# Kernel optimization log

Measured on AMD Instinct MI355X. Metric: run time of the kernel, lower is better.

Reference implementation:

```python
import jax, jax.numpy as jnp
import numpy as np

H = 1024      # hidden_size
V = 50257     # output_size (vocab)
L = 100       # max_length


def setup_inputs() -> dict:
    key = jax.random.key(0)
    ks = jax.random.split(key, 14)
    s = 0.02
    return {
        "token": jax.random.randint(ks[0], (1,), 0, V),
        "hidden": jax.random.normal(ks[1], (1, 1, H), jnp.float32),
        "encoder_outputs": jax.random.normal(ks[2], (L, H), jnp.float32),
        "embedding": jax.random.normal(ks[3], (V, H), jnp.float32) * s,
        "attn_w": jax.random.normal(ks[4], (L, 2 * H), jnp.float32) * s,
        "attn_b": jnp.zeros((L,), jnp.float32),
        "comb_w": jax.random.normal(ks[5], (H, 2 * H), jnp.float32) * s,
        "comb_b": jnp.zeros((H,), jnp.float32),
        "w_ih": jax.random.normal(ks[6], (3 * H, H), jnp.float32) * s,
        "w_hh": jax.random.normal(ks[7], (3 * H, H), jnp.float32) * s,
        "b_ih": jnp.zeros((3 * H,), jnp.float32),
        "b_hh": jnp.zeros((3 * H,), jnp.float32),
        "out_w": jax.random.normal(ks[8], (V, H), jnp.float32) * s,
        "out_b": jnp.zeros((V,), jnp.float32),
    }


def reference(token, hidden, encoder_outputs, embedding, attn_w, attn_b,
              comb_w, comb_b, w_ih, w_hh, b_ih, b_hh, out_w, out_b):
    # embedding lookup; dropout is identity in eval mode
    emb = embedding[token]                                   # [1, H]
    h0 = hidden[0]                                           # [1, H]
    # attention over encoder positions
    attn_in = jnp.concatenate([emb, h0], axis=1)             # [1, 2H]
    attn_weights = jax.nn.softmax(attn_in @ attn_w.T + attn_b, axis=1)  # [1, L]
    attn_applied = attn_weights @ encoder_outputs            # [1, H]
    # combine + relu
    x = jnp.concatenate([emb, attn_applied], axis=1) @ comb_w.T + comb_b  # [1, H]
    x = jax.nn.relu(x)
    # single GRU cell step (PyTorch gate order: r, z, n)
    gi = x @ w_ih.T + b_ih                                   # [1, 3H]
    gh = h0 @ w_hh.T + b_hh                                  # [1, 3H]
    ir, iz, in_ = jnp.split(gi, 3, axis=1)
    hr, hz, hn = jnp.split(gh, 3, axis=1)
    r = jax.nn.sigmoid(ir + hr)
    z = jax.nn.sigmoid(iz + hz)
    n = jnp.tanh(in_ + r * hn)
    h_new = (1.0 - z) * n + z * h0                           # [1, H]
    # output projection + log_softmax
    output = jax.nn.log_softmax(h_new @ out_w.T + out_b, axis=1)  # [1, V]
    return output, h_new[None], attn_weights
```

## Files before the change

### kernel.cpp

```cpp
#include <hip/hip_runtime.h>
#include <hip/hip_bf16.h>

#define H 1024
#define V 50257
#define L 100
#define NPART 1024


__device__ __forceinline__ float block_reduce_sum_256(float v, float* sbuf4) {
    #pragma unroll
    for (int off = 32; off > 0; off >>= 1)
        v += __shfl_down(v, off, 64);
    int lane = threadIdx.x & 63;
    int wid  = threadIdx.x >> 6;
    __syncthreads();
    if (lane == 0) sbuf4[wid] = v;
    __syncthreads();
    return sbuf4[0] + sbuf4[1] + sbuf4[2] + sbuf4[3];
}


__global__ void k1_logits_gh(const int* token, const float* hidden, const float* embedding,
                             const float* attn_w, const float* attn_b,
                             const float* w_hh, const float* b_hh,
                             float* ws_log, float* ws_gh) {
    __shared__ float sbuf[4];
    int b = blockIdx.x;
    if (b < L) {
        int tok = token[0];
        const float* emb = embedding + (size_t)tok * H;
        const float* wrow = attn_w + (size_t)b * (2 * H);
        float acc = 0.f;
        for (int k = threadIdx.x; k < 2 * H; k += 256) {
            float inv = (k < H) ? emb[k] : hidden[k - H];
            acc += inv * wrow[k];
        }
        float s = block_reduce_sum_256(acc, sbuf);
        if (threadIdx.x == 0) ws_log[b] = s + attn_b[b];
    } else {
        int rb = b - L;
        float4 hv = ((const float4*)hidden)[threadIdx.x];
        #pragma unroll
        for (int i = 0; i < 4; i++) {
            int r = rb * 4 + i;
            const float4* wr = (const float4*)(w_hh + (size_t)r * H);
            float4 w = wr[threadIdx.x];
            float acc = w.x * hv.x + w.y * hv.y + w.z * hv.z + w.w * hv.w;
            float s = block_reduce_sum_256(acc, sbuf);
            if (threadIdx.x == 0) ws_gh[r] = s + b_hh[r];
        }
    }
}


__global__ void k2_softmax_apply(const float* ws_log, const float* enc,
                                 float* ws_app, float* out_attnw) {
    __shared__ float wsm[L];
    if (threadIdx.x < L) wsm[threadIdx.x] = ws_log[threadIdx.x];
    __syncthreads();
    float m = -1e30f;
    for (int l = 0; l < L; l++) m = fmaxf(m, wsm[l]);
    float s = 0.f;
    for (int l = 0; l < L; l++) s += expf(wsm[l] - m);
    __syncthreads();
    if (threadIdx.x < L) wsm[threadIdx.x] = expf(wsm[threadIdx.x] - m) / s;
    __syncthreads();
    int h = blockIdx.x * 256 + threadIdx.x;
    float acc = 0.f;
    for (int l = 0; l < L; l++) acc += wsm[l] * enc[l * H + h];
    ws_app[h] = acc;
    if (blockIdx.x == 0 && threadIdx.x < L) out_attnw[threadIdx.x] = wsm[threadIdx.x];
}


__global__ void k3_combine(const int* token, const float* embedding, const float* ws_app,
                           const float* comb_w, const float* comb_b, float* ws_x) {
    __shared__ float sbuf[4];
    int tok = token[0];
    const float* emb = embedding + (size_t)tok * H;
    float4 e = ((const float4*)emb)[threadIdx.x];
    float4 a = ((const float4*)ws_app)[threadIdx.x];
    for (int r = blockIdx.x; r < H; r += gridDim.x) {
        const float4* wr = (const float4*)(comb_w + (size_t)r * (2 * H));
        float4 w0 = wr[threadIdx.x];
        float4 w1 = wr[256 + threadIdx.x];
        float acc = w0.x * e.x + w0.y * e.y + w0.z * e.z + w0.w * e.w
                  + w1.x * a.x + w1.y * a.y + w1.z * a.z + w1.w * a.w;
        float s = block_reduce_sum_256(acc, sbuf);
        if (threadIdx.x == 0) ws_x[r] = fmaxf(s + comb_b[r], 0.0f);
    }
}


__global__ void k4_gi(const float* ws_x, const float* w_ih, const float* b_ih, float* ws_gi) {
    __shared__ float sbuf[4];
    float4 xv = ((const float4*)ws_x)[threadIdx.x];
    for (int r = blockIdx.x; r < 3 * H; r += gridDim.x) {
        const float4* wr = (const float4*)(w_ih + (size_t)r * H);
        float4 w = wr[threadIdx.x];
        float acc = w.x * xv.x + w.y * xv.y + w.z * xv.z + w.w * xv.w;
        float s = block_reduce_sum_256(acc, sbuf);
        if (threadIdx.x == 0) ws_gi[r] = s + b_ih[r];
    }
}


__global__ void k5_gates(const float* ws_gi, const float* ws_gh, const float* hidden,
                         float* out_h, float* ws_hn) {
    int h = blockIdx.x * 256 + threadIdx.x;
    float ir = ws_gi[h], iz = ws_gi[H + h], in_ = ws_gi[2 * H + h];
    float hr = ws_gh[h], hz = ws_gh[H + h], hn = ws_gh[2 * H + h];
    float r = 1.f / (1.f + expf(-(ir + hr)));
    float z = 1.f / (1.f + expf(-(iz + hz)));
    float n = tanhf(in_ + r * hn);
    float h0 = hidden[h];
    float v = (1.f - z) * n + z * h0;
    out_h[h] = v;
    ws_hn[h] = v;
}


__global__ void k6_outproj(const float* hn, const float* out_w, const float* out_b,
                           float* out_logits, float* ws_pm, float* ws_ps) {
    __shared__ float sm[4], ss[4];
    int lane = threadIdx.x & 63;
    int wv   = threadIdx.x >> 6;
    const float4* h4 = (const float4*)hn;
    float4 h0 = h4[lane], h1 = h4[lane + 64], h2 = h4[lane + 128], h3 = h4[lane + 192];
    float m = -1e30f, s = 0.f;
    int wid = blockIdx.x * 4 + wv;
    for (int r = wid; r < V; r += NPART * 4) {
        const float4* wr = (const float4*)(out_w + (size_t)r * H);
        float4 a = wr[lane], b = wr[lane + 64], c = wr[lane + 128], d = wr[lane + 192];
        float acc = a.x * h0.x + a.y * h0.y + a.z * h0.z + a.w * h0.w
                  + b.x * h1.x + b.y * h1.y + b.z * h1.z + b.w * h1.w
                  + c.x * h2.x + c.y * h2.y + c.z * h2.z + c.w * h2.w
                  + d.x * h3.x + d.y * h3.y + d.z * h3.z + d.w * h3.w;
        #pragma unroll
        for (int off = 32; off > 0; off >>= 1) acc += __shfl_down(acc, off, 64);
        if (lane == 0) {
            float lg = acc + out_b[r];
            out_logits[r] = lg;
            float nm = fmaxf(m, lg);
            s = s * expf(m - nm) + expf(lg - nm);
            m = nm;
        }
    }
    if (lane == 0) { sm[wv] = m; ss[wv] = s; }
    __syncthreads();
    if (threadIdx.x == 0) {
        m = sm[0]; s = ss[0];
        for (int i = 1; i < 4; i++) {
            float nm = fmaxf(m, sm[i]);
            s = s * expf(m - nm) + ss[i] * expf(sm[i] - nm);
            m = nm;
        }
        ws_pm[blockIdx.x] = m;
        ws_ps[blockIdx.x] = s;
    }
}


__global__ void k7_finalize(const float* ws_pm, const float* ws_ps, float* out) {
    __shared__ float sm[4], ss[4], fm, fs;
    int t = threadIdx.x;
    float m = -1e30f, s = 0.f;
    for (int i = t; i < NPART; i += 256) {
        float pm = ws_pm[i], ps = ws_ps[i];
        float nm = fmaxf(m, pm);
        s = s * expf(m - nm) + ps * expf(pm - nm);
        m = nm;
    }
    #pragma unroll
    for (int off = 32; off > 0; off >>= 1) {
        float om = __shfl_down(m, off, 64);
        float os = __shfl_down(s, off, 64);
        float nm = fmaxf(m, om);
        s = s * expf(m - nm) + os * expf(om - nm);
        m = nm;
    }
    int lane = t & 63, wv = t >> 6;
    if (lane == 0) { sm[wv] = m; ss[wv] = s; }
    __syncthreads();
    if (t == 0) {
        m = sm[0]; s = ss[0];
        for (int i = 1; i < 4; i++) {
            float nm = fmaxf(m, sm[i]);
            s = s * expf(m - nm) + ss[i] * expf(sm[i] - nm);
            m = nm;
        }
        fm = m; fs = logf(s);
    }
    __syncthreads();
    float M = fm, LS = fs;
    for (int v = blockIdx.x * 256 + t; v < V; v += gridDim.x * 256)
        out[v] = out[v] - M - LS;
}


extern "C" void kernel_launch(void* const* d_in, const int* in_sizes, int n_in,
                              void* d_out, int out_size, void* d_ws, size_t ws_size,
                              hipStream_t stream) {
    const int*   token     = (const int*)d_in[0];
    const float* hidden    = (const float*)d_in[1];
    const float* enc       = (const float*)d_in[2];
    const float* embedding = (const float*)d_in[3];
    const float* attn_w    = (const float*)d_in[4];
    const float* attn_b    = (const float*)d_in[5];
    const float* comb_w    = (const float*)d_in[6];
    const float* comb_b    = (const float*)d_in[7];
    const float* w_ih      = (const float*)d_in[8];
    const float* w_hh      = (const float*)d_in[9];
    const float* b_ih      = (const float*)d_in[10];
    const float* b_hh      = (const float*)d_in[11];
    const float* out_w     = (const float*)d_in[12];
    const float* out_b     = (const float*)d_in[13];

    float* out = (float*)d_out;
    float* ws  = (float*)d_ws;
    float* ws_log = ws;
    float* ws_app = ws + 128;
    float* ws_x   = ws + 1152;
    float* ws_gi  = ws + 2176;
    float* ws_gh  = ws + 5248;
    float* ws_pm  = ws + 8320;
    float* ws_ps  = ws + 9344;
    float* ws_hn  = ws + 10368;

    k1_logits_gh<<<dim3(L + 768), dim3(256), 0, stream>>>(token, hidden, embedding,
                                                          attn_w, attn_b, w_hh, b_hh,
                                                          ws_log, ws_gh);
    k2_softmax_apply<<<dim3(4), dim3(256), 0, stream>>>(ws_log, enc, ws_app, out + V + H);
    k3_combine<<<dim3(256), dim3(256), 0, stream>>>(token, embedding, ws_app,
                                                    comb_w, comb_b, ws_x);
    k4_gi<<<dim3(768), dim3(256), 0, stream>>>(ws_x, w_ih, b_ih, ws_gi);
    k5_gates<<<dim3(4), dim3(256), 0, stream>>>(ws_gi, ws_gh, hidden, out + V, ws_hn);
    k6_outproj<<<dim3(NPART), dim3(256), 0, stream>>>(ws_hn, out_w, out_b, out, ws_pm, ws_ps);
    k7_finalize<<<dim3(64), dim3(256), 0, stream>>>(ws_pm, ws_ps, out);
}
```

Before: 67.63 us.

## Fuse decoder stages into five kernels with wave-per-row GEMVs and fused GRU gates

Cuts the kernel count from seven to five. The attention softmax, attention apply and combine projection are fused into one kernel, with each block recomputing the attention-applied vector into shared memory. The w_ih and w_hh GEMVs are merged with the gate math in one kernel, one wavefront per hidden unit. All GEMVs now use one 64-lane wavefront per row with shuffle reduction instead of 256-thread block reductions and syncthreads, and the output projection handles two rows per wave per iteration. The aim is to remove launch overhead and synchronisation on this latency-bound decode step, at the cost of recomputing the attention-applied vector (100x1024 encoder reads) in each of 128 blocks.

```diff
diff --git a/kernel.cpp b/kernel.cpp
--- a/kernel.cpp
+++ b/kernel.cpp
@@ -7,120 +7,125 @@
 #define NPART 1024
 
 
-__device__ __forceinline__ float block_reduce_sum_256(float v, float* sbuf4) {
-    #pragma unroll
-    for (int off = 32; off > 0; off >>= 1)
-        v += __shfl_down(v, off, 64);
-    int lane = threadIdx.x & 63;
-    int wid  = threadIdx.x >> 6;
-    __syncthreads();
-    if (lane == 0) sbuf4[wid] = v;
-    __syncthreads();
-    return sbuf4[0] + sbuf4[1] + sbuf4[2] + sbuf4[3];
-}
-
-
-__global__ void k1_logits_gh(const int* token, const float* hidden, const float* embedding,
-                             const float* attn_w, const float* attn_b,
-                             const float* w_hh, const float* b_hh,
-                             float* ws_log, float* ws_gh) {
-    __shared__ float sbuf[4];
-    int b = blockIdx.x;
-    if (b < L) {
-        int tok = token[0];
-        const float* emb = embedding + (size_t)tok * H;
-        const float* wrow = attn_w + (size_t)b * (2 * H);
+__global__ void kA_logits(const int* token, const float* hidden, const float* embedding,
+                          const float* attn_w, const float* attn_b, float* ws_log) {
+    int lane = threadIdx.x;
+    int r = blockIdx.x;
+    const float4* e4 = (const float4*)(embedding + (size_t)token[0] * H);
+    const float4* h4 = (const float4*)hidden;
+    const float4* wr = (const float4*)(attn_w + (size_t)r * (2 * H));
+    float acc = 0.f;
+    #pragma unroll
+    for (int j = 0; j < 4; j++) {
+        float4 w = wr[lane + 64 * j];
+        float4 v = e4[lane + 64 * j];
+        acc += w.x * v.x + w.y * v.y + w.z * v.z + w.w * v.w;
+    }
+    #pragma unroll
+    for (int j = 0; j < 4; j++) {
+        float4 w = wr[256 + lane + 64 * j];
+        float4 v = h4[lane + 64 * j];
+        acc += w.x * v.x + w.y * v.y + w.z * v.z + w.w * v.w;
+    }
+    #pragma unroll
+    for (int off = 32; off > 0; off >>= 1) acc += __shfl_down(acc, off, 64);
+    if (lane == 0) ws_log[r] = acc + attn_b[r];
+}
+
+
+__global__ void kB_softmax_combine(const int* token, const float* ws_log, const float* enc,
+                                   const float* embedding, const float* comb_w,
+                                   const float* comb_b, float* ws_x, float* out_attnw) {
+    __shared__ float lg_s[L];
+    __shared__ float aw_s[L];
+    __shared__ float app_s[H];
+    int t = threadIdx.x;
+    if (t < L) lg_s[t] = ws_log[t];
+    __syncthreads();
+    float m = -1e30f;
+    for (int l = 0; l < L; l++) m = fmaxf(m, lg_s[l]);
+    float s = 0.f;
+    for (int l = 0; l < L; l++) s += expf(lg_s[l] - m);
+    if (t < L) aw_s[t] = expf(lg_s[t] - m) / s;
+    __syncthreads();
+    for (int h = t; h < H; h += 256) {
+        float a = 0.f;
+        for (int l = 0; l < L; l++) a += aw_s[l] * enc[l * H + h];
+        app_s[h] = a;
+    }
+    if (blockIdx.x == 0 && t < L) out_attnw[t] = aw_s[t];
+    __syncthreads();
+    int lane = t & 63, wv = t >> 6;
+    const float4* e4 = (const float4*)(embedding + (size_t)token[0] * H);
+    const float4* a4 = (const float4*)app_s;
+    #pragma unroll
+    for (int i = 0; i < 2; i++) {
+        int r = blockIdx.x * 8 + wv * 2 + i;
+        const float4* wr = (const float4*)(comb_w + (size_t)r * (2 * H));
         float acc = 0.f;
-        for (int k = threadIdx.x; k < 2 * H; k += 256) {
-            float inv = (k < H) ? emb[k] : hidden[k - H];
-            acc += inv * wrow[k];
-        }
-        float s = block_reduce_sum_256(acc, sbuf);
-        if (threadIdx.x == 0) ws_log[b] = s + attn_b[b];
-    } else {
-        int rb = b - L;
-        float4 hv = ((const float4*)hidden)[threadIdx.x];
-        #pragma unroll
-        for (int i = 0; i < 4; i++) {
-            int r = rb * 4 + i;
-            const float4* wr = (const float4*)(w_hh + (size_t)r * H);
-            float4 w = wr[threadIdx.x];
-            float acc = w.x * hv.x + w.y * hv.y + w.z * hv.z + w.w * hv.w;
-            float s = block_reduce_sum_256(acc, sbuf);
-            if (threadIdx.x == 0) ws_gh[r] = s + b_hh[r];
-        }
-    }
-}
-
-
-__global__ void k2_softmax_apply(const float* ws_log, const float* enc,
-                                 float* ws_app, float* out_attnw) {
-    __shared__ float wsm[L];
-    if (threadIdx.x < L) wsm[threadIdx.x] = ws_log[threadIdx.x];
-    __syncthreads();
-    float m = -1e30f;
-    for (int l = 0; l < L; l++) m = fmaxf(m, wsm[l]);
-    float s = 0.f;
-    for (int l = 0; l < L; l++) s += expf(wsm[l] - m);
-    __syncthreads();
-    if (threadIdx.x < L) wsm[threadIdx.x] = expf(wsm[threadIdx.x] - m) / s;
-    __syncthreads();
-    int h = blockIdx.x * 256 + threadIdx.x;
-    float acc = 0.f;
-    for (int l = 0; l < L; l++) acc += wsm[l] * enc[l * H + h];
-    ws_app[h] = acc;
-    if (blockIdx.x == 0 && threadIdx.x < L) out_attnw[threadIdx.x] = wsm[threadIdx.x];
-}
-
-
-__global__ void k3_combine(const int* token, const float* embedding, const float* ws_app,
-                           const float* comb_w, const float* comb_b, float* ws_x) {
-    __shared__ float sbuf[4];
-    int tok = token[0];
-    const float* emb = embedding + (size_t)tok * H;
-    float4 e = ((const float4*)emb)[threadIdx.x];
-    float4 a = ((const float4*)ws_app)[threadIdx.x];
-    for (int r = blockIdx.x; r < H; r += gridDim.x) {
-        const float4* wr = (const float4*)(comb_w + (size_t)r * (2 * H));
-        float4 w0 = wr[threadIdx.x];
-        float4 w1 = wr[256 + threadIdx.x];
-        float acc = w0.x * e.x + w0.y * e.y + w0.z * e.z + w0.w * e.w
-                  + w1.x * a.x + w1.y * a.y + w1.z * a.z + w1.w * a.w;
-        float s = block_reduce_sum_256(acc, sbuf);
-        if (threadIdx.x == 0) ws_x[r] = fmaxf(s + comb_b[r], 0.0f);
-    }
-}
-
-
-__global__ void k4_gi(const float* ws_x, const float* w_ih, const float* b_ih, float* ws_gi) {
-    __shared__ float sbuf[4];
-    float4 xv = ((const float4*)ws_x)[threadIdx.x];
-    for (int r = blockIdx.x; r < 3 * H; r += gridDim.x) {
-        const float4* wr = (const float4*)(w_ih + (size_t)r * H);
-        float4 w = wr[threadIdx.x];
-        float acc = w.x * xv.x + w.y * xv.y + w.z * xv.z + w.w * xv.w;
-        float s = block_reduce_sum_256(acc, sbuf);
-        if (threadIdx.x == 0) ws_gi[r] = s + b_ih[r];
-    }
-}
-
-
-__global__ void k5_gates(const float* ws_gi, const float* ws_gh, const float* hidden,
-                         float* out_h, float* ws_hn) {
-    int h = blockIdx.x * 256 + threadIdx.x;
-    float ir = ws_gi[h], iz = ws_gi[H + h], in_ = ws_gi[2 * H + h];
-    float hr = ws_gh[h], hz = ws_gh[H + h], hn = ws_gh[2 * H + h];
-    float r = 1.f / (1.f + expf(-(ir + hr)));
-    float z = 1.f / (1.f + expf(-(iz + hz)));
-    float n = tanhf(in_ + r * hn);
-    float h0 = hidden[h];
-    float v = (1.f - z) * n + z * h0;
-    out_h[h] = v;
-    ws_hn[h] = v;
-}
-
-
-__global__ void k6_outproj(const float* hn, const float* out_w, const float* out_b,
+        #pragma unroll
+        for (int j = 0; j < 4; j++) {
+            float4 w = wr[lane + 64 * j];
+            float4 v = e4[lane + 64 * j];
+            acc += w.x * v.x + w.y * v.y + w.z * v.z + w.w * v.w;
+        }
+        #pragma unroll
+        for (int j = 0; j < 4; j++) {
+            float4 w = wr[256 + lane + 64 * j];
+            float4 v = a4[lane + 64 * j];
+            acc += w.x * v.x + w.y * v.y + w.z * v.z + w.w * v.w;
+        }
+        #pragma unroll
+        for (int off = 32; off > 0; off >>= 1) acc += __shfl_down(acc, off, 64);
+        if (lane == 0) ws_x[r] = fmaxf(acc + comb_b[r], 0.0f);
+    }
+}
+
+
+__global__ void kC_gru(const float* ws_x, const float* hidden,
+                       const float* w_ih, const float* w_hh,
+                       const float* b_ih, const float* b_hh,
+                       float* out_h, float* ws_hn) {
+    int lane = threadIdx.x & 63, wv = threadIdx.x >> 6;
+    int h = blockIdx.x * 4 + wv;
+    const float4* x4 = (const float4*)ws_x;
+    const float4* h4 = (const float4*)hidden;
+    float acc[6] = {0.f, 0.f, 0.f, 0.f, 0.f, 0.f};
+    #pragma unroll
+    for (int j = 0; j < 4; j++) {
+        float4 xv = x4[lane + 64 * j];
+        float4 hv = h4[lane + 64 * j];
+        #pragma unroll
+        for (int k = 0; k < 3; k++) {
+            float4 w = ((const float4*)(w_ih + (size_t)(k * H + h) * H))[lane + 64 * j];
+            acc[k] += w.x * xv.x + w.y * xv.y + w.z * xv.z + w.w * xv.w;
+        }
+        #pragma unroll
+        for (int k = 0; k < 3; k++) {
+            float4 w = ((const float4*)(w_hh + (size_t)(k * H + h) * H))[lane + 64 * j];
+            acc[3 + k] += w.x * hv.x + w.y * hv.y + w.z * hv.z + w.w * hv.w;
+        }
+    }
+    #pragma unroll
+    for (int off = 32; off > 0; off >>= 1) {
+        #pragma unroll
+        for (int k = 0; k < 6; k++) acc[k] += __shfl_down(acc[k], off, 64);
+    }
+    if (lane == 0) {
+        float ir = acc[0] + b_ih[h], iz = acc[1] + b_ih[H + h], in_ = acc[2] + b_ih[2 * H + h];
+        float hr = acc[3] + b_hh[h], hz = acc[4] + b_hh[H + h], hn = acc[5] + b_hh[2 * H + h];
+        float r = 1.f / (1.f + expf(-(ir + hr)));
+        float z = 1.f / (1.f + expf(-(iz + hz)));
+        float n = tanhf(in_ + r * hn);
+        float h0 = hidden[h];
+        float v = (1.f - z) * n + z * h0;
+        out_h[h] = v;
+        ws_hn[h] = v;
+    }
+}
+
+
+__global__ void kD_outproj(const float* hn, const float* out_w, const float* out_b,
                            float* out_logits, float* ws_pm, float* ws_ps) {
     __shared__ float sm[4], ss[4];
     int lane = threadIdx.x & 63;
@@ -129,27 +134,48 @@
     float4 h0 = h4[lane], h1 = h4[lane + 64], h2 = h4[lane + 128], h3 = h4[lane + 192];
     float m = -1e30f, s = 0.f;
     int wid = blockIdx.x * 4 + wv;
-    for (int r = wid; r < V; r += NPART * 4) {
-        const float4* wr = (const float4*)(out_w + (size_t)r * H);
-        float4 a = wr[lane], b = wr[lane + 64], c = wr[lane + 128], d = wr[lane + 192];
-        float acc = a.x * h0.x + a.y * h0.y + a.z * h0.z + a.w * h0.w
-                  + b.x * h1.x + b.y * h1.y + b.z * h1.z + b.w * h1.w
-                  + c.x * h2.x + c.y * h2.y + c.z * h2.z + c.w * h2.w
-                  + d.x * h3.x + d.y * h3.y + d.z * h3.z + d.w * h3.w;
-        #pragma unroll
-        for (int off = 32; off > 0; off >>= 1) acc += __shfl_down(acc, off, 64);
+    for (int r0 = wid * 2; r0 < V; r0 += NPART * 8) {
+        const float4* wr0 = (const float4*)(out_w + (size_t)r0 * H);
+        float4 a = wr0[lane], b = wr0[lane + 64], c = wr0[lane + 128], d = wr0[lane + 192];
+        float acc0 = a.x * h0.x + a.y * h0.y + a.z * h0.z + a.w * h0.w
+                   + b.x * h1.x + b.y * h1.y + b.z * h1.z + b.w * h1.w
+                   + c.x * h2.x + c.y * h2.y + c.z * h2.z + c.w * h2.w
+                   + d.x * h3.x + d.y * h3.y + d.z * h3.z + d.w * h3.w;
+        bool have2 = (r0 + 1) < V;
+        float acc1 = 0.f;
+        if (have2) {
+            const float4* wr1 = (const float4*)(out_w + (size_t)(r0 + 1) * H);
+            float4 e = wr1[lane], f = wr1[lane + 64], g = wr1[lane + 128], k = wr1[lane + 192];
+            acc1 = e.x * h0.x + e.y * h0.y + e.z * h0.z + e.w * h0.w
+                 + f.x * h1.x + f.y * h1.y + f.z * h1.z + f.w * h1.w
+                 + g.x * h2.x + g.y * h2.y + g.z * h2.z + g.w * h2.w
+                 + k.x * h3.x + k.y * h3.y + k.z * h3.z + k.w * h3.w;
+        }
+        #pragma unroll
+        for (int off = 32; off > 0; off >>= 1) {
+            acc0 += __shfl_down(acc0, off, 64);
+            acc1 += __shfl_down(acc1, off, 64);
+        }
         if (lane == 0) {
-            float lg = acc + out_b[r];
-            out_logits[r] = lg;
+            float lg = acc0 + out_b[r0];
+            out_logits[r0] = lg;
             float nm = fmaxf(m, lg);
             s = s * expf(m - nm) + expf(lg - nm);
             m = nm;
+            if (have2) {
+                float lg1 = acc1 + out_b[r0 + 1];
+                out_logits[r0 + 1] = lg1;
+                nm = fmaxf(m, lg1);
+                s = s * expf(m - nm) + expf(lg1 - nm);
+                m = nm;
+            }
         }
     }
     if (lane == 0) { sm[wv] = m; ss[wv] = s; }
     __syncthreads();
     if (threadIdx.x == 0) {
         m = sm[0]; s = ss[0];
+        #pragma unroll
         for (int i = 1; i < 4; i++) {
             float nm = fmaxf(m, sm[i]);
             s = s * expf(m - nm) + ss[i] * expf(sm[i] - nm);
@@ -161,7 +187,7 @@
 }
 
 
-__global__ void k7_finalize(const float* ws_pm, const float* ws_ps, float* out) {
+__global__ void kE_finalize(const float* ws_pm, const float* ws_ps, float* out) {
     __shared__ float sm[4], ss[4], fm, fs;
     int t = threadIdx.x;
     float m = -1e30f, s = 0.f;
@@ -184,6 +210,7 @@
     __syncthreads();
     if (t == 0) {
         m = sm[0]; s = ss[0];
+        #pragma unroll
         for (int i = 1; i < 4; i++) {
             float nm = fmaxf(m, sm[i]);
             s = s * expf(m - nm) + ss[i] * expf(sm[i] - nm);
@@ -219,22 +246,17 @@
     float* out = (float*)d_out;
     float* ws  = (float*)d_ws;
     float* ws_log = ws;
-    float* ws_app = ws + 128;
-    float* ws_x   = ws + 1152;
-    float* ws_gi  = ws + 2176;
-    float* ws_gh  = ws + 5248;
-    float* ws_pm  = ws + 8320;
-    float* ws_ps  = ws + 9344;
-    float* ws_hn  = ws + 10368;
-
-    k1_logits_gh<<<dim3(L + 768), dim3(256), 0, stream>>>(token, hidden, embedding,
-                                                          attn_w, attn_b, w_hh, b_hh,
-                                                          ws_log, ws_gh);
-    k2_softmax_apply<<<dim3(4), dim3(256), 0, stream>>>(ws_log, enc, ws_app, out + V + H);
-    k3_combine<<<dim3(256), dim3(256), 0, stream>>>(token, embedding, ws_app,
-                                                    comb_w, comb_b, ws_x);
-    k4_gi<<<dim3(768), dim3(256), 0, stream>>>(ws_x, w_ih, b_ih, ws_gi);
-    k5_gates<<<dim3(4), dim3(256), 0, stream>>>(ws_gi, ws_gh, hidden, out + V, ws_hn);
-    k6_outproj<<<dim3(NPART), dim3(256), 0, stream>>>(ws_hn, out_w, out_b, out, ws_pm, ws_ps);
-    k7_finalize<<<dim3(64), dim3(256), 0, stream>>>(ws_pm, ws_ps, out);
-}
+    float* ws_x   = ws + 128;
+    float* ws_pm  = ws + 1152;
+    float* ws_ps  = ws + 2176;
+    float* ws_hn  = ws + 3200;
+
+    kA_logits<<<dim3(L), dim3(64), 0, stream>>>(token, hidden, embedding,
+                                                attn_w, attn_b, ws_log);
+    kB_softmax_combine<<<dim3(128), dim3(256), 0, stream>>>(token, ws_log, enc, embedding,
+                                                            comb_w, comb_b, ws_x, out + V + H);
+    kC_gru<<<dim3(256), dim3(256), 0, stream>>>(ws_x, hidden, w_ih, w_hh, b_ih, b_hh,
+                                                out + V, ws_hn);
+    kD_outproj<<<dim3(NPART), dim3(256), 0, stream>>>(ws_hn, out_w, out_b, out, ws_pm, ws_ps);
+    kE_finalize<<<dim3(128), dim3(256), 0, stream>>>(ws_pm, ws_ps, out);
+}
```

Result: slower. 145.2 us (+114.7%).
